# Kernel tuning notes

Measured on AMD Instinct MI355X. Metric: run time of the kernel, lower is better.

## Reference

```python
import jax, jax.numpy as jnp
import numpy as np

EPS = 1e-6
BETA = 0.5
B, T, N = 128, 30, 10000   # batch, BP iterations, n error bits
M, K = 5000, 10            # checks, observables
CHK_W, OBS_W = 6, 50       # row weights of chkmat / obsmat


def _make_supports():
    """Deterministic sparse supports (CSR-style flattened col indices + row ids)."""
    rng = np.random.default_rng(0)
    chk_rows = np.argpartition(rng.random((M, N)), CHK_W, axis=1)[:, :CHK_W]
    obs_rows = np.argpartition(rng.random((K, N)), OBS_W, axis=1)[:, :OBS_W]
    chk_idx = chk_rows.reshape(-1).astype(np.int32)
    chk_seg = np.repeat(np.arange(M, dtype=np.int32), CHK_W)
    obs_idx = obs_rows.reshape(-1).astype(np.int32)
    obs_seg = np.repeat(np.arange(K, dtype=np.int32), OBS_W)
    return chk_idx, chk_seg, obs_idx, obs_seg


def setup_inputs() -> dict:
    key = jax.random.key(0)
    k1, k2, k3 = jax.random.split(key, 3)
    all_llrs = jax.random.normal(k1, (B, T, N), dtype=jnp.float32) * 2.0
    syndromes = jax.random.randint(k2, (B, M), 0, 2, dtype=jnp.int32)
    observables = jax.random.randint(k3, (B, K), 0, 2, dtype=jnp.int32)
    chk_idx, chk_seg, obs_idx, obs_seg = _make_supports()
    return {
        "all_llrs": all_llrs,
        "syndromes": syndromes,
        "observables": observables,
        "chk_idx": jnp.asarray(chk_idx),
        "chk_seg": jnp.asarray(chk_seg),
        "obs_idx": jnp.asarray(obs_idx),
        "obs_seg": jnp.asarray(obs_seg),
    }


def _pred_llr(t, idx, seg, num_seg):
    # t: (B,T,N) tanh(llr/2); gather support cols -> (B,T,E)
    g = t[:, :, idx]
    # segmented product over support entries (tanh rule), segments on axis 0
    p = jax.ops.segment_prod(jnp.moveaxis(g, 2, 0), seg, num_segments=num_seg)  # (S,B,T)
    p = jnp.clip(jnp.moveaxis(p, 0, 2), -1.0 + EPS, 1.0 - EPS)  # (B,T,S)
    return 2.0 * jnp.arctanh(p)


def _bce_with_logits(z, y):
    # stable BCEWithLogits: max(z,0) - z*y + log(1+exp(-|z|)) == logaddexp(0,z) - z*y
    return jnp.logaddexp(0.0, z) - z * y


def reference(all_llrs, syndromes, observables, chk_idx, chk_seg, obs_idx, obs_seg):
    t = jnp.tanh(all_llrs * 0.5)                                   # (B,T,N)
    syn_llr = _pred_llr(t, chk_idx, chk_seg, syndromes.shape[1])    # (B,T,M)
    obs_llr = _pred_llr(t, obs_idx, obs_seg, observables.shape[1])  # (B,T,K)
    y_syn = syndromes.astype(jnp.float32)[:, None, :]
    y_obs = observables.astype(jnp.float32)[:, None, :]
    loss1 = _bce_with_logits(-syn_llr, y_syn).sum(axis=2)           # (B,T)
    loss2 = _bce_with_logits(-obs_llr, y_obs).sum(axis=2)           # (B,T)
    loss = BETA * loss1 + (1.0 - BETA) * loss2
    return loss.mean()
```

## Files before the change

### kernel.cpp

```cpp
#include <hip/hip_runtime.h>

typedef float floatx2 __attribute__((ext_vector_type(2)));

#define B_  128
#define T_  30
#define N_  10000
#define M_  5000
#define K_  10
#define OBS_W_ 50
#define EPS_ 1e-6f
#define LOG2F_ 0.69314718056f
#define BT_  3840
#define BTP_ 4096
#define CHUNK_ 40
#define NCHK_ (M_/CHUNK_)

__global__ __launch_bounds__(256) void tanh_transpose_fp8(
    const float*   __restrict__ llrs,
    unsigned char* __restrict__ tt)
{
    __shared__ float tile[64][65];
    const int bt0 = blockIdx.x * 64;
    const int n0  = blockIdx.y * 64;
    const int tid = threadIdx.x;
    const int c   = tid & 63;
    const int r4  = tid >> 6;

    if (n0 + c < N_) {
        #pragma unroll
        for (int i = 0; i < 16; ++i) {
            int r = i * 4 + r4;
            float v = llrs[(size_t)(bt0 + r) * N_ + (n0 + c)];
            tile[r][c] = 1.f - 2.f / (__expf(v) + 1.f);
        }
    }
    __syncthreads();

    const int pair = tid & 31;
    const int colg = tid >> 5;
    const int r    = bt0 + 2 * pair;
    const int bb   = r / 30;
    const int pr   = bb * 32 + (r - bb * 30);
    #pragma unroll
    for (int i = 0; i < 8; ++i) {
        int col = colg + 8 * i;
        if (n0 + col < N_) {
            float v0 = tile[2 * pair][col];
            float v1 = tile[2 * pair + 1][col];
            int pk = __builtin_amdgcn_cvt_pk_fp8_f32(v0, v1, 0, false);
            *(unsigned short*)(tt + (size_t)(n0 + col) * BTP_ + pr) =
                (unsigned short)pk;
        }
    }
}

__device__ __forceinline__ void fold8(uint2 q, float* p, bool first) {
    floatx2 a0 = __builtin_amdgcn_cvt_pk_f32_fp8((int)q.x, false);
    floatx2 a1 = __builtin_amdgcn_cvt_pk_f32_fp8((int)q.x, true);
    floatx2 a2 = __builtin_amdgcn_cvt_pk_f32_fp8((int)q.y, false);
    floatx2 a3 = __builtin_amdgcn_cvt_pk_f32_fp8((int)q.y, true);
    if (first) {
        p[0] = a0.x; p[1] = a0.y; p[2] = a1.x; p[3] = a1.y;
        p[4] = a2.x; p[5] = a2.y; p[6] = a3.x; p[7] = a3.y;
    } else {
        p[0] *= a0.x; p[1] *= a0.y; p[2] *= a1.x; p[3] *= a1.y;
        p[4] *= a2.x; p[5] *= a2.y; p[6] *= a3.x; p[7] *= a3.y;
    }
}

__global__ __launch_bounds__(256) void gather_loss_fp8(
    const unsigned char* __restrict__ tt,
    const int*           __restrict__ syndromes,
    const int*           __restrict__ observables,
    const int*           __restrict__ chk_idx,
    const int*           __restrict__ obs_idx,
    float*               __restrict__ out)
{
    const int tid  = threadIdx.x;
    const int lane = tid & 63;
    const int wave = tid >> 6;
    const int r0   = blockIdx.x * 512 + lane * 8;
    const int b    = r0 >> 5;
    const int roff = r0 >> 3;
    const float pmask = ((r0 & 31) == 24) ? 0.f : 1.f;
    const uint2* tt2 = (const uint2*)tt;

    float acc = 0.f;
    const int y = blockIdx.y;

    if (y < NCHK_) {
        const int* syn = syndromes + (size_t)b * M_;
        const int m0 = y * CHUNK_ + wave * (CHUNK_ / 4);
        #pragma unroll 2
        for (int m = m0; m < m0 + CHUNK_ / 4; ++m) {
            const int* ci = chk_idx + m * 6;
            uint2 q0 = tt2[(size_t)ci[0] * (BTP_ / 8) + roff];
            uint2 q1 = tt2[(size_t)ci[1] * (BTP_ / 8) + roff];
            uint2 q2 = tt2[(size_t)ci[2] * (BTP_ / 8) + roff];
            uint2 q3 = tt2[(size_t)ci[3] * (BTP_ / 8) + roff];
            uint2 q4 = tt2[(size_t)ci[4] * (BTP_ / 8) + roff];
            uint2 q5 = tt2[(size_t)ci[5] * (BTP_ / 8) + roff];
            float p[8];
            fold8(q0, p, true);  fold8(q1, p, false); fold8(q2, p, false);
            fold8(q3, p, false); fold8(q4, p, false); fold8(q5, p, false);
            const float sgn = syn[m] ? -1.f : 1.f;
            float local = 0.f;
            #pragma unroll
            for (int j = 0; j < 8; ++j) {
                float sp = sgn * p[j];
                sp = fminf(fmaxf(sp, -1.f + EPS_), 1.f - EPS_);
                float tm = LOG2F_ - __logf(1.f + sp);
                local += (j < 6) ? tm : tm * pmask;
            }
            acc += local;
        }
    } else {
        const int* ob = observables + (size_t)b * K_;
        for (int k = wave; k < K_; k += 4) {
            const int* oi = obs_idx + k * OBS_W_;
            float p[8];
            uint2 q = tt2[(size_t)oi[0] * (BTP_ / 8) + roff];
            fold8(q, p, true);
            #pragma unroll 7
            for (int j2 = 1; j2 < OBS_W_; ++j2) {
                uint2 qq = tt2[(size_t)oi[j2] * (BTP_ / 8) + roff];
                fold8(qq, p, false);
            }
            const float sgn = ob[k] ? -1.f : 1.f;
            float local = 0.f;
            #pragma unroll
            for (int j = 0; j < 8; ++j) {
                float sp = sgn * p[j];
                sp = fminf(fmaxf(sp, -1.f + EPS_), 1.f - EPS_);
                float tm = LOG2F_ - __logf(1.f + sp);
                local += (j < 6) ? tm : tm * pmask;
            }
            acc += local;
        }
    }

    __shared__ float red[4];
    #pragma unroll
    for (int off = 32; off > 0; off >>= 1)
        acc += __shfl_down(acc, off, 64);
    if (lane == 0) red[wave] = acc;
    __syncthreads();
    if (tid == 0) {
        float s = red[0] + red[1] + red[2] + red[3];
        atomicAdd(out, s * (0.5f / (float)BT_));
    }
}

extern "C" void kernel_launch(void* const* d_in, const int* in_sizes, int n_in,
                              void* d_out, int out_size, void* d_ws, size_t ws_size,
                              hipStream_t stream) {
    const float* all_llrs    = (const float*)d_in[0];
    const int*   syndromes   = (const int*)d_in[1];
    const int*   observables = (const int*)d_in[2];
    const int*   chk_idx     = (const int*)d_in[3];
    const int*   obs_idx     = (const int*)d_in[5];
    float*         out = (float*)d_out;
    unsigned char* tt  = (unsigned char*)d_ws;

    hipMemsetAsync(out, 0, sizeof(float) * out_size, stream);

    dim3 g1(BT_ / 64, (N_ + 63) / 64);
    tanh_transpose_fp8<<<g1, 256, 0, stream>>>(all_llrs, tt);

    dim3 g2(BTP_ / 512, NCHK_ + 1);
    gather_loss_fp8<<<g2, 256, 0, stream>>>(
        tt, syndromes, observables, chk_idx, obs_idx, out);
}
```

Baseline: 285.7 us.

## Drop padded fp8 layout, vectorize transpose, stage check indices and syndromes in LDS

The transposed fp8 tanh buffer now uses an unpadded BT stride of 3840 instead of padding each batch to 32 rows. This removes the wasted gather bandwidth and the masked lanes. The transpose reads float4 and writes packed 4-byte fp8 words. The gather kernel handles 4 rows per lane, covers 100 checks per block, and loads the check indices and per-batch syndromes into shared memory first. In exchange, each lane may straddle two batches, so it needs per-element sign selection, and the gathers become narrower 4-byte loads.

```diff
diff --git a/kernel.cpp b/kernel.cpp
--- a/kernel.cpp
+++ b/kernel.cpp
@@ -11,9 +11,9 @@
 #define EPS_ 1e-6f
 #define LOG2F_ 0.69314718056f
 #define BT_  3840
-#define BTP_ 4096
-#define CHUNK_ 40
+#define CHUNK_ 100
 #define NCHK_ (M_/CHUNK_)
+#define NB_ 10
 
 __global__ __launch_bounds__(256) void tanh_transpose_fp8(
     const float*   __restrict__ llrs,
@@ -23,49 +23,43 @@
     const int bt0 = blockIdx.x * 64;
     const int n0  = blockIdx.y * 64;
     const int tid = threadIdx.x;
-    const int c   = tid & 63;
-    const int r4  = tid >> 6;
 
-    if (n0 + c < N_) {
-        #pragma unroll
-        for (int i = 0; i < 16; ++i) {
-            int r = i * 4 + r4;
-            float v = llrs[(size_t)(bt0 + r) * N_ + (n0 + c)];
-            tile[r][c] = 1.f - 2.f / (__expf(v) + 1.f);
+    #pragma unroll
+    for (int i = 0; i < 4; ++i) {
+        int lin = i * 256 + tid;
+        int r   = lin >> 4;
+        int c4  = (lin & 15) * 4;
+        if (n0 + c4 < N_) {
+            float4 v = *(const float4*)(llrs + (size_t)(bt0 + r) * N_ + n0 + c4);
+            tile[r][c4 + 0] = 1.f - 2.f / (__expf(v.x) + 1.f);
+            tile[r][c4 + 1] = 1.f - 2.f / (__expf(v.y) + 1.f);
+            tile[r][c4 + 2] = 1.f - 2.f / (__expf(v.z) + 1.f);
+            tile[r][c4 + 3] = 1.f - 2.f / (__expf(v.w) + 1.f);
         }
     }
     __syncthreads();
 
-    const int pair = tid & 31;
-    const int colg = tid >> 5;
-    const int r    = bt0 + 2 * pair;
-    const int bb   = r / 30;
-    const int pr   = bb * 32 + (r - bb * 30);
+    const int q  = tid & 15;
+    const int cg = tid >> 4;
     #pragma unroll
-    for (int i = 0; i < 8; ++i) {
-        int col = colg + 8 * i;
+    for (int i = 0; i < 4; ++i) {
+        int col = cg + 16 * i;
         if (n0 + col < N_) {
-            float v0 = tile[2 * pair][col];
-            float v1 = tile[2 * pair + 1][col];
+            float v0 = tile[4 * q + 0][col];
+            float v1 = tile[4 * q + 1][col];
+            float v2 = tile[4 * q + 2][col];
+            float v3 = tile[4 * q + 3][col];
             int pk = __builtin_amdgcn_cvt_pk_fp8_f32(v0, v1, 0, false);
-            *(unsigned short*)(tt + (size_t)(n0 + col) * BTP_ + pr) =
-                (unsigned short)pk;
+            pk     = __builtin_amdgcn_cvt_pk_fp8_f32(v2, v3, pk, true);
+            *(int*)(tt + (size_t)(n0 + col) * BT_ + bt0 + 4 * q) = pk;
         }
     }
 }
 
-__device__ __forceinline__ void fold8(uint2 q, float* p, bool first) {
-    floatx2 a0 = __builtin_amdgcn_cvt_pk_f32_fp8((int)q.x, false);
-    floatx2 a1 = __builtin_amdgcn_cvt_pk_f32_fp8((int)q.x, true);
-    floatx2 a2 = __builtin_amdgcn_cvt_pk_f32_fp8((int)q.y, false);
-    floatx2 a3 = __builtin_amdgcn_cvt_pk_f32_fp8((int)q.y, true);
-    if (first) {
-        p[0] = a0.x; p[1] = a0.y; p[2] = a1.x; p[3] = a1.y;
-        p[4] = a2.x; p[5] = a2.y; p[6] = a3.x; p[7] = a3.y;
-    } else {
-        p[0] *= a0.x; p[1] *= a0.y; p[2] *= a1.x; p[3] *= a1.y;
-        p[4] *= a2.x; p[5] *= a2.y; p[6] *= a3.x; p[7] *= a3.y;
-    }
+__device__ __forceinline__ void cvt4(unsigned int qv, float* a) {
+    floatx2 lo = __builtin_amdgcn_cvt_pk_f32_fp8((int)qv, false);
+    floatx2 hi = __builtin_amdgcn_cvt_pk_f32_fp8((int)qv, true);
+    a[0] = lo.x; a[1] = lo.y; a[2] = hi.x; a[3] = hi.y;
 }
 
 __global__ __launch_bounds__(256) void gather_loss_fp8(
@@ -76,70 +70,85 @@
     const int*           __restrict__ obs_idx,
     float*               __restrict__ out)
 {
+    __shared__ int   sidx[CHUNK_ * 6];
+    __shared__ int   ssyn[NB_][CHUNK_];
+    __shared__ float red[4];
+
     const int tid  = threadIdx.x;
     const int lane = tid & 63;
     const int wave = tid >> 6;
-    const int r0   = blockIdx.x * 512 + lane * 8;
-    const int b    = r0 >> 5;
-    const int roff = r0 >> 3;
-    const float pmask = ((r0 & 31) == 24) ? 0.f : 1.f;
-    const uint2* tt2 = (const uint2*)tt;
-
+    const int r0   = blockIdx.x * 256 + lane * 4;
+    const int bA   = r0 / 30;
+    const int bB   = (r0 + 3) / 30;
+    const int split= (bA + 1) * 30 - r0;
+    const int b_lo = (blockIdx.x * 256) / 30;
+    const unsigned char* col0 = tt + r0;
+    const int y = blockIdx.y;
     float acc = 0.f;
-    const int y = blockIdx.y;
 
     if (y < NCHK_) {
-        const int* syn = syndromes + (size_t)b * M_;
-        const int m0 = y * CHUNK_ + wave * (CHUNK_ / 4);
+        const int m0 = y * CHUNK_;
+        for (int i = tid; i < CHUNK_ * 6; i += 256)
+            sidx[i] = chk_idx[m0 * 6 + i];
+        for (int i = tid; i < NB_ * CHUNK_; i += 256) {
+            int bi = i / CHUNK_, j = i - bi * CHUNK_;
+            int b  = b_lo + bi; if (b > B_ - 1) b = B_ - 1;
+            ((int*)ssyn)[i] = syndromes[(size_t)b * M_ + m0 + j];
+        }
+        __syncthreads();
+        const int iA = bA - b_lo, iB = bB - b_lo;
+
         #pragma unroll 2
-        for (int m = m0; m < m0 + CHUNK_ / 4; ++m) {
-            const int* ci = chk_idx + m * 6;
-            uint2 q0 = tt2[(size_t)ci[0] * (BTP_ / 8) + roff];
-            uint2 q1 = tt2[(size_t)ci[1] * (BTP_ / 8) + roff];
-            uint2 q2 = tt2[(size_t)ci[2] * (BTP_ / 8) + roff];
-            uint2 q3 = tt2[(size_t)ci[3] * (BTP_ / 8) + roff];
-            uint2 q4 = tt2[(size_t)ci[4] * (BTP_ / 8) + roff];
-            uint2 q5 = tt2[(size_t)ci[5] * (BTP_ / 8) + roff];
-            float p[8];
-            fold8(q0, p, true);  fold8(q1, p, false); fold8(q2, p, false);
-            fold8(q3, p, false); fold8(q4, p, false); fold8(q5, p, false);
-            const float sgn = syn[m] ? -1.f : 1.f;
-            float local = 0.f;
+        for (int s = wave * 25; s < wave * 25 + 25; ++s) {
+            int i0 = sidx[s * 6 + 0], i1 = sidx[s * 6 + 1], i2 = sidx[s * 6 + 2];
+            int i3 = sidx[s * 6 + 3], i4 = sidx[s * 6 + 4], i5 = sidx[s * 6 + 5];
+            unsigned int q0 = *(const unsigned int*)(col0 + (size_t)i0 * BT_);
+            unsigned int q1 = *(const unsigned int*)(col0 + (size_t)i1 * BT_);
+            unsigned int q2 = *(const unsigned int*)(col0 + (size_t)i2 * BT_);
+            unsigned int q3 = *(const unsigned int*)(col0 + (size_t)i3 * BT_);
+            unsigned int q4 = *(const unsigned int*)(col0 + (size_t)i4 * BT_);
+            unsigned int q5 = *(const unsigned int*)(col0 + (size_t)i5 * BT_);
+            float a[4], b4[4], p[4];
+            cvt4(q0, p);  cvt4(q1, a);  cvt4(q2, b4);
             #pragma unroll
-            for (int j = 0; j < 8; ++j) {
-                float sp = sgn * p[j];
+            for (int j = 0; j < 4; ++j) p[j] *= a[j] * b4[j];
+            cvt4(q3, a);  cvt4(q4, b4);
+            #pragma unroll
+            for (int j = 0; j < 4; ++j) p[j] *= a[j] * b4[j];
+            cvt4(q5, a);
+            float sgA = ssyn[iA][s] ? -1.f : 1.f;
+            float sgB = ssyn[iB][s] ? -1.f : 1.f;
+            #pragma unroll
+            for (int j = 0; j < 4; ++j) {
+                float sg = (j >= split) ? sgB : sgA;
+                float sp = sg * p[j] * a[j];
                 sp = fminf(fmaxf(sp, -1.f + EPS_), 1.f - EPS_);
-                float tm = LOG2F_ - __logf(1.f + sp);
-                local += (j < 6) ? tm : tm * pmask;
+                acc += LOG2F_ - __logf(1.f + sp);
             }
-            acc += local;
         }
     } else {
-        const int* ob = observables + (size_t)b * K_;
         for (int k = wave; k < K_; k += 4) {
             const int* oi = obs_idx + k * OBS_W_;
-            float p[8];
-            uint2 q = tt2[(size_t)oi[0] * (BTP_ / 8) + roff];
-            fold8(q, p, true);
-            #pragma unroll 7
-            for (int j2 = 1; j2 < OBS_W_; ++j2) {
-                uint2 qq = tt2[(size_t)oi[j2] * (BTP_ / 8) + roff];
-                fold8(qq, p, false);
+            float p[4] = {1.f, 1.f, 1.f, 1.f};
+            #pragma unroll 5
+            for (int j2 = 0; j2 < OBS_W_; ++j2) {
+                unsigned int qq = *(const unsigned int*)(col0 + (size_t)oi[j2] * BT_);
+                float a[4];
+                cvt4(qq, a);
+                p[0] *= a[0]; p[1] *= a[1]; p[2] *= a[2]; p[3] *= a[3];
             }
-            const float sgn = ob[k] ? -1.f : 1.f;
-            float local = 0.f;
+            float sgA = observables[(size_t)bA * K_ + k] ? -1.f : 1.f;
+            float sgB = observables[(size_t)bB * K_ + k] ? -1.f : 1.f;
             #pragma unroll
-            for (int j = 0; j < 8; ++j) {
-                float sp = sgn * p[j];
+            for (int j = 0; j < 4; ++j) {
+                float sg = (j >= split) ? sgB : sgA;
+                float sp = sg * p[j];
                 sp = fminf(fmaxf(sp, -1.f + EPS_), 1.f - EPS_);
-                float tm = LOG2F_ - __logf(1.f + sp);
-                local += (j < 6) ? tm : tm * pmask;
+                acc += LOG2F_ - __logf(1.f + sp);
             }
-            acc += local;
         }
     }
 
-    __shared__ float red[4];
     #pragma unroll
     for (int off = 32; off > 0; off >>= 1)
         acc += __shfl_down(acc, off, 64);
@@ -167,7 +176,7 @@
     dim3 g1(BT_ / 64, (N_ + 63) / 64);
     tanh_transpose_fp8<<<g1, 256, 0, stream>>>(all_llrs, tt);
 
-    dim3 g2(BTP_ / 512, NCHK_ + 1);
+    dim3 g2(BT_ / 256, NCHK_ + 1);
     gather_loss_fp8<<<g2, 256, 0, stream>>>(
         tt, syndromes, observables, chk_idx, obs_idx, out);
 }
```

After: 275.4 us. 3.6% less time.
